# Kernel tuning notes

Hardware: AMD Instinct MI355X
Metric: run time of the kernel (lower is better)

The kernel has to match this reference:

```python
import jax, jax.numpy as jnp
import numpy as np

EMBED_DIM = 512
NUM_HEADS = 8
HEAD_DIM = EMBED_DIM // NUM_HEADS
N_NODES = 65536
EPS = 1e-5


def setup_inputs() -> dict:
    key = jax.random.key(0)
    ks = jax.random.split(key, 16)
    std = 0.02
    E, F = EMBED_DIM, 4 * EMBED_DIM
    return {
        "x": jax.random.normal(ks[0], (N_NODES, E), jnp.float32),
        "Wq": jax.random.normal(ks[1], (E, E), jnp.float32) * std,
        "bq": jnp.zeros((E,), jnp.float32),
        "Wk": jax.random.normal(ks[2], (E, E), jnp.float32) * std,
        "bk": jnp.zeros((E,), jnp.float32),
        "Wv": jax.random.normal(ks[3], (E, E), jnp.float32) * std,
        "bv": jnp.zeros((E,), jnp.float32),
        "Wo": jax.random.normal(ks[4], (E, E), jnp.float32) * std,
        "bo": jnp.zeros((E,), jnp.float32),
        "W1": jax.random.normal(ks[5], (F, E), jnp.float32) * std,
        "b1": jnp.zeros((F,), jnp.float32),
        "W2": jax.random.normal(ks[6], (E, F), jnp.float32) * std,
        "b2": jnp.zeros((E,), jnp.float32),
        "g1": jnp.ones((E,), jnp.float32),
        "beta1": jnp.zeros((E,), jnp.float32),
        "g2": jnp.ones((E,), jnp.float32),
        "beta2": jnp.zeros((E,), jnp.float32),
    }


def _layernorm(x, g, b):
    mu = jnp.mean(x, axis=-1, keepdims=True)
    var = jnp.mean(jnp.square(x - mu), axis=-1, keepdims=True)
    return (x - mu) * jax.lax.rsqrt(var + EPS) * g + b


def reference(x, Wq, bq, Wk, bk, Wv, bv, Wo, bo, W1, b1, W2, b2, g1, beta1, g2, beta2):
    N = x.shape[0]
    H, D = NUM_HEADS, HEAD_DIM
    residual = x
    h = _layernorm(x, g1, beta1)
    q = (h @ Wq.T + bq).reshape(N, H, D)
    k = (h @ Wk.T + bk).reshape(N, H, D)
    v = (h @ Wv.T + bv).reshape(N, H, D)
    # per-node attention across heads: scores (N, H, H)
    scores = jnp.einsum('nhd,ngd->nhg', q, k) / np.float32(np.sqrt(D))
    attn = jax.nn.softmax(scores, axis=-1)
    out = jnp.einsum('nhg,ngd->nhd', attn, v).reshape(N, H * D)
    out = out @ Wo.T + bo
    x = residual + out  # dropout is identity in eval
    residual = x
    h = _layernorm(x, g2, beta2)
    ff = jax.nn.relu(h @ W1.T + b1) @ W2.T + b2
    return residual + ff
```

## Files before the change

### kernel.cpp

```cpp
#include <hip/hip_runtime.h>
#include <hip/hip_bf16.h>
#include <stdint.h>

typedef __hip_bfloat16 bf16;
typedef short bf16x8 __attribute__((ext_vector_type(8)));
typedef float f32x4 __attribute__((ext_vector_type(4)));

typedef __attribute__((address_space(1))) const unsigned int as1_uint;
typedef __attribute__((address_space(3))) unsigned int as3_uint;

__device__ __forceinline__ void async_copy16(const void* g, void* l) {
    __builtin_amdgcn_global_load_lds((as1_uint*)g, (as3_uint*)l, 16, 0, 0);
}

__device__ __forceinline__ float b2f(unsigned short u) {
    union { unsigned int i; float f; } c; c.i = ((unsigned int)u) << 16; return c.f;
}
__device__ __forceinline__ unsigned short f2b(float f) {
    union { float f; unsigned int i; } c; c.f = f;
    unsigned int i = c.i;
    i += 0x7fffu + ((i >> 16) & 1u);
    return (unsigned short)(i >> 16);
}

__global__ __launch_bounds__(256)
void cvt_kernel(const float* __restrict__ in, bf16* __restrict__ out)
{
    const int i = (blockIdx.x * 256 + threadIdx.x) * 8;
    const float4 a = *(const float4*)(in + i);
    const float4 b = *(const float4*)(in + i + 4);
    union { uint4 v; unsigned short s[8]; } u;
    u.s[0] = f2b(a.x); u.s[1] = f2b(a.y); u.s[2] = f2b(a.z); u.s[3] = f2b(a.w);
    u.s[4] = f2b(b.x); u.s[5] = f2b(b.y); u.s[6] = f2b(b.z); u.s[7] = f2b(b.w);
    *(uint4*)((unsigned short*)out + i) = u.v;
}

__global__ __launch_bounds__(256)
void ln_kernel(const float* __restrict__ x, const float* __restrict__ g,
               const float* __restrict__ beta, bf16* __restrict__ out)
{
    const int w = threadIdx.x >> 6, l = threadIdx.x & 63;
    const int n = blockIdx.x * 4 + w;

    const float* xr = x + (size_t)n * 512 + l * 8;
    const float4 a = *(const float4*)xr;
    const float4 b = *(const float4*)(xr + 4);
    float f[8] = {a.x, a.y, a.z, a.w, b.x, b.y, b.z, b.w};

    float s = 0.f, q = 0.f;
#pragma unroll
    for (int i = 0; i < 8; ++i) { s += f[i]; q += f[i] * f[i]; }
#pragma unroll
    for (int o = 32; o > 0; o >>= 1) { s += __shfl_xor(s, o); q += __shfl_xor(q, o); }
    const float mean = s * (1.f / 512.f);
    const float var  = q * (1.f / 512.f) - mean * mean;
    const float rstd = rsqrtf(var + 1e-5f);

    const float4 g0 = *(const float4*)(g + l * 8);
    const float4 g1 = *(const float4*)(g + l * 8 + 4);
    const float4 b0 = *(const float4*)(beta + l * 8);
    const float4 b1 = *(const float4*)(beta + l * 8 + 4);
    const float gg[8] = {g0.x,g0.y,g0.z,g0.w,g1.x,g1.y,g1.z,g1.w};
    const float bb[8] = {b0.x,b0.y,b0.z,b0.w,b1.x,b1.y,b1.z,b1.w};

    union { uint4 v; unsigned short s[8]; } o;
#pragma unroll
    for (int i = 0; i < 8; ++i)
        o.s[i] = f2b((f[i] - mean) * rstd * gg[i] + bb[i]);
    *(uint4*)((unsigned short*)out + (size_t)n * 512 + l * 8) = o.v;
}

__global__ __launch_bounds__(256)
void attn_kernel(const bf16* __restrict__ qkv, bf16* __restrict__ out)
{
    __shared__ unsigned short sm[4][1536];
    const int w = threadIdx.x >> 6, l = threadIdx.x & 63;
    const int n = blockIdx.x * 4 + w;

    const uint4* src = (const uint4*)((const unsigned short*)qkv + (size_t)n * 1536);
    uint4* dst = (uint4*)sm[w];
#pragma unroll
    for (int i = 0; i < 3; ++i) dst[i * 64 + l] = src[i * 64 + l];
    __syncthreads();

    const int h = l >> 3, gi = l & 7;
    const unsigned short* qrow = sm[w] + h * 64;
    const unsigned short* krow = sm[w] + 512 + gi * 64;
    float s = 0.f;
#pragma unroll
    for (int jj = 0; jj < 8; ++jj) {
        union { uint4 v; unsigned short s8[8]; } qa, ka;
        qa.v = *(const uint4*)(qrow + jj * 8);
        ka.v = *(const uint4*)(krow + jj * 8);
#pragma unroll
        for (int j = 0; j < 8; ++j) s += b2f(qa.s8[j]) * b2f(ka.s8[j]);
    }
    s *= 0.125f;

    float m = s;
#pragma unroll
    for (int o = 1; o < 8; o <<= 1) m = fmaxf(m, __shfl_xor(m, o));
    float e = __expf(s - m);
    float d = e;
#pragma unroll
    for (int o = 1; o < 8; o <<= 1) d += __shfl_xor(d, o);
    const float p = e / d;

    float acc[8];
#pragma unroll
    for (int j = 0; j < 8; ++j) acc[j] = 0.f;
    const int j8 = (l & 7) * 8;
#pragma unroll
    for (int gg = 0; gg < 8; ++gg) {
        const float pg = __shfl(p, (l & 56) | gg);
        union { uint4 v; unsigned short s8[8]; } va;
        va.v = *(const uint4*)(sm[w] + 1024 + gg * 64 + j8);
#pragma unroll
        for (int j = 0; j < 8; ++j) acc[j] += pg * b2f(va.s8[j]);
    }
    union { uint4 v; unsigned short s8[8]; } o;
#pragma unroll
    for (int j = 0; j < 8; ++j) o.s8[j] = f2b(acc[j]);
    *(uint4*)((unsigned short*)out + (size_t)n * 512 + h * 64 + j8) = o.v;
}

#define EPI_PLAIN 0
#define EPI_RES   1
#define EPI_RELU  2

template<int MODE>
__global__ __launch_bounds__(256)
void gemm_bt(const bf16* __restrict__ A,
             const bf16* __restrict__ B0, const bf16* __restrict__ B1,
             const bf16* __restrict__ B2,
             const float* __restrict__ bias0, const float* __restrict__ bias1,
             const float* __restrict__ bias2,
             const float* __restrict__ res,
             void* __restrict__ C,
             int K, int Nper, int ldc)
{
    __shared__ bf16 As[128 * 64];
    __shared__ bf16 Bs[128 * 64];

    const int tid = threadIdx.x;
    const int w = tid >> 6, l = tid & 63;
    const int rowBase = blockIdx.y * 128;
    const int colBase = blockIdx.x * 128;
    const int sel = colBase / Nper;
    const bf16*  B    = (sel == 0) ? B0 : (sel == 1) ? B1 : B2;
    const float* bias = (sel == 0) ? bias0 : (sel == 1) ? bias1 : bias2;
    const int colInB = colBase - sel * Nper;

    const int la = l >> 3;
    const int lk = (l & 7) * 8;
    const bf16* Ag = A + (size_t)(rowBase + w * 32 + la) * K + lk;
    const bf16* Bg = B + (size_t)(colInB + w * 32 + la) * K + lk;
    bf16* AsW = As + (w * 32) * 64;
    bf16* BsW = Bs + (w * 32) * 64;

    const int wr = w >> 1, wc = w & 1;
    const int ml = l & 15;
    const int kq = (l >> 4) * 8;

    f32x4 acc[4][4];
#pragma unroll
    for (int i = 0; i < 4; ++i)
#pragma unroll
        for (int j = 0; j < 4; ++j) acc[i][j] = (f32x4)(0.f);

    for (int k0 = 0; k0 < K; k0 += 64) {
#pragma unroll
        for (int i = 0; i < 4; ++i) {
            async_copy16(Ag + (size_t)(i * 8) * K + k0, AsW + i * 8 * 64);
            async_copy16(Bg + (size_t)(i * 8) * K + k0, BsW + i * 8 * 64);
        }
        __syncthreads();
#pragma unroll
        for (int kk = 0; kk < 2; ++kk) {
            const int ko = kk * 32 + kq;
            bf16x8 af[4], bfr[4];
#pragma unroll
            for (int mi = 0; mi < 4; ++mi)
                af[mi] = *(const bf16x8*)(As + (wr * 64 + mi * 16 + ml) * 64 + ko);
#pragma unroll
            for (int ni = 0; ni < 4; ++ni)
                bfr[ni] = *(const bf16x8*)(Bs + (wc * 64 + ni * 16 + ml) * 64 + ko);
#pragma unroll
            for (int mi = 0; mi < 4; ++mi)
#pragma unroll
                for (int ni = 0; ni < 4; ++ni)
                    acc[mi][ni] = __builtin_amdgcn_mfma_f32_16x16x32_bf16(
                        af[mi], bfr[ni], acc[mi][ni], 0, 0, 0);
        }
        __syncthreads();
    }

    float bv[4];
#pragma unroll
    for (int ni = 0; ni < 4; ++ni)
        bv[ni] = bias[colInB + wc * 64 + ni * 16 + ml];

#pragma unroll
    for (int mi = 0; mi < 4; ++mi) {
#pragma unroll
        for (int r = 0; r < 4; ++r) {
            const int row = rowBase + wr * 64 + mi * 16 + (l >> 4) * 4 + r;
            const size_t rowoff = (size_t)row * ldc;
#pragma unroll
            for (int ni = 0; ni < 4; ++ni) {
                const int gcol = colBase + wc * 64 + ni * 16 + ml;
                float v = acc[mi][ni][r] + bv[ni];
                if (MODE == EPI_RELU) v = fmaxf(v, 0.f);
                if (MODE == EPI_RES) {
                    v += res[rowoff + gcol];
                    ((float*)C)[rowoff + gcol] = v;
                } else {
                    ((unsigned short*)C)[rowoff + gcol] = f2b(v);
                }
            }
        }
    }
}

extern "C" void kernel_launch(void* const* d_in, const int* in_sizes, int n_in,
                              void* d_out, int out_size, void* d_ws, size_t ws_size,
                              hipStream_t stream)
{
    const float* x   = (const float*)d_in[0];
    const float* Wq  = (const float*)d_in[1];
    const float* bq  = (const float*)d_in[2];
    const float* Wk  = (const float*)d_in[3];
    const float* bk  = (const float*)d_in[4];
    const float* Wv  = (const float*)d_in[5];
    const float* bv  = (const float*)d_in[6];
    const float* Wo  = (const float*)d_in[7];
    const float* bo  = (const float*)d_in[8];
    const float* W1  = (const float*)d_in[9];
    const float* b1  = (const float*)d_in[10];
    const float* W2  = (const float*)d_in[11];
    const float* b2  = (const float*)d_in[12];
    const float* g1  = (const float*)d_in[13];
    const float* be1 = (const float*)d_in[14];
    const float* g2  = (const float*)d_in[15];
    const float* be2 = (const float*)d_in[16];

    const int N = 65536;

    bf16* Wqb = (bf16*)d_ws;
    bf16* Wkb = Wqb + 262144;
    bf16* Wvb = Wkb + 262144;
    bf16* Wob = Wvb + 262144;
    bf16* W1b = Wob + 262144;
    bf16* W2b = W1b + 1048576;
    const size_t wts_bytes = 6ull * 1024 * 1024;
    bf16* t64 = (bf16*)((char*)d_ws + wts_bytes);
    const size_t t64_bytes = (size_t)N * 512 * 2;
    bf16* cb  = (bf16*)((char*)d_ws + wts_bytes + t64_bytes);
    const size_t used = wts_bytes + t64_bytes;
    const size_t avail = ws_size > used ? ws_size - used : 0;
    int Nc = N;
    while (Nc > 128 && (size_t)Nc * 4096 > avail) Nc >>= 1;

    float* x2 = (float*)d_out;
    dim3 blk(256);

    cvt_kernel<<<262144 / 2048, blk, 0, stream>>>(Wq, Wqb);
    cvt_kernel<<<262144 / 2048, blk, 0, stream>>>(Wk, Wkb);
    cvt_kernel<<<262144 / 2048, blk, 0, stream>>>(Wv, Wvb);
    cvt_kernel<<<262144 / 2048, blk, 0, stream>>>(Wo, Wob);
    cvt_kernel<<<1048576 / 2048, blk, 0, stream>>>(W1, W1b);
    cvt_kernel<<<1048576 / 2048, blk, 0, stream>>>(W2, W2b);

    ln_kernel<<<N / 4, blk, 0, stream>>>(x, g1, be1, t64);

    for (int r0 = 0; r0 < N; r0 += Nc) {
        gemm_bt<EPI_PLAIN><<<dim3(12, Nc / 128), blk, 0, stream>>>(
            t64 + (size_t)r0 * 512, Wqb, Wkb, Wvb, bq, bk, bv, nullptr,
            cb, 512, 512, 1536);
        attn_kernel<<<Nc / 4, blk, 0, stream>>>(cb, t64 + (size_t)r0 * 512);
    }

    gemm_bt<EPI_RES><<<dim3(4, N / 128), blk, 0, stream>>>(
        t64, Wob, Wob, Wob, bo, bo, bo, x, x2, 512, 512, 512);

    ln_kernel<<<N / 4, blk, 0, stream>>>(x2, g2, be2, t64);

    for (int r0 = 0; r0 < N; r0 += Nc) {
        gemm_bt<EPI_RELU><<<dim3(16, Nc / 128), blk, 0, stream>>>(
            t64 + (size_t)r0 * 512, W1b, W1b, W1b, b1, b1, b1, nullptr,
            cb, 512, 2048, 2048);
        gemm_bt<EPI_RES><<<dim3(4, Nc / 128), blk, 0, stream>>>(
            cb, W2b, W2b, W2b, b2, b2, b2, x2 + (size_t)r0 * 512,
            x2 + (size_t)r0 * 512, 2048, 512, 512);
    }
}
```

Before: 1.076 ms.

## Rewrite GEMM as 256x256 tile with 4-stage async LDS pipeline and XCD remap

The bf16 GEMM moves from 128x128 tiles with 4 waves and a single LDS buffer to 256x256 tiles with 8 waves. Global-to-LDS loads run through a 4-slot ring with K-step 32 and a prefetch depth of 3, paced by explicit vmcnt waits, and the LDS layout uses an XOR swizzle to avoid bank conflicts. Workgroup IDs are remapped so neighbouring tiles share an XCD, and MFMA sections raise wave priority. The aim is to hide load latency and raise data reuse, at the cost of more LDS (128KB) and registers per block, and a different chunk size for the host loop.

Result: faster. 1.052 ms (-2.3%).

```diff
diff --git a/kernel.cpp b/kernel.cpp
--- a/kernel.cpp
+++ b/kernel.cpp
@@ -129,7 +129,7 @@
 #define EPI_RELU  2
 
 template<int MODE>
-__global__ __launch_bounds__(256)
+__global__ __launch_bounds__(512, 2)
 void gemm_bt(const bf16* __restrict__ A,
              const bf16* __restrict__ B0, const bf16* __restrict__ B1,
              const bf16* __restrict__ B2,
@@ -139,77 +139,104 @@
              void* __restrict__ C,
              int K, int Nper, int ldc)
 {
-    __shared__ bf16 As[128 * 64];
-    __shared__ bf16 Bs[128 * 64];
+    __shared__ bf16 As[4][8192];
+    __shared__ bf16 Bs[4][8192];
 
     const int tid = threadIdx.x;
     const int w = tid >> 6, l = tid & 63;
-    const int rowBase = blockIdx.y * 128;
-    const int colBase = blockIdx.x * 128;
+
+    const int nbx = gridDim.x;
+    const int nwg = nbx * (int)gridDim.y;
+    int lid = blockIdx.y * nbx + blockIdx.x;
+    {
+        const int q = nwg >> 3, r = nwg & 7;
+        const int xcd = lid & 7, idx = lid >> 3;
+        lid = (xcd < r ? xcd * (q + 1) : r * (q + 1) + (xcd - r) * q) + idx;
+    }
+    const int bx = lid % nbx, by = lid / nbx;
+
+    const int rowBase = by * 256;
+    const int colBase = bx * 256;
     const int sel = colBase / Nper;
     const bf16*  B    = (sel == 0) ? B0 : (sel == 1) ? B1 : B2;
     const float* bias = (sel == 0) ? bias0 : (sel == 1) ? bias1 : bias2;
     const int colInB = colBase - sel * Nper;
 
-    const int la = l >> 3;
-    const int lk = (l & 7) * 8;
-    const bf16* Ag = A + (size_t)(rowBase + w * 32 + la) * K + lk;
-    const bf16* Bg = B + (size_t)(colInB + w * 32 + la) * K + lk;
-    bf16* AsW = As + (w * 32) * 64;
-    bf16* BsW = Bs + (w * 32) * 64;
-
-    const int wr = w >> 1, wc = w & 1;
+    const bf16* Ag = A + (size_t)rowBase * K;
+    const bf16* Bg = B + (size_t)colInB * K;
+
+    const int wr = w >> 2, wc = w & 3;
     const int ml = l & 15;
-    const int kq = (l >> 4) * 8;
-
-    f32x4 acc[4][4];
-#pragma unroll
-    for (int i = 0; i < 4; ++i)
+    const int kc = l >> 4;
+    const int ac = ((kc ^ ((ml >> 1) & 3)) << 3);
+
+    auto stage = [&](int t, int slot) {
+        const int lr = l >> 2, lc = l & 3;
+#pragma unroll
+        for (int j = 0; j < 2; ++j) {
+            const int cid = w * 2 + j;
+            const int r = (cid << 4) + lr;
+            const int c = lc ^ ((lr >> 1) & 3);
+            const size_t go = (size_t)r * K + (t << 5) + (c << 3);
+            async_copy16(Ag + go, &As[slot][cid << 9]);
+            async_copy16(Bg + go, &Bs[slot][cid << 9]);
+        }
+    };
+
+    f32x4 acc[8][4];
+#pragma unroll
+    for (int i = 0; i < 8; ++i)
 #pragma unroll
         for (int j = 0; j < 4; ++j) acc[i][j] = (f32x4)(0.f);
 
-    for (int k0 = 0; k0 < K; k0 += 64) {
-#pragma unroll
-        for (int i = 0; i < 4; ++i) {
-            async_copy16(Ag + (size_t)(i * 8) * K + k0, AsW + i * 8 * 64);
-            async_copy16(Bg + (size_t)(i * 8) * K + k0, BsW + i * 8 * 64);
+    const int NT = K >> 5;
+
+    stage(0, 0); stage(1, 1); stage(2, 2);
+    asm volatile("s_waitcnt vmcnt(8)" ::: "memory");
+    __builtin_amdgcn_s_barrier();
+
+    for (int t = 0; t < NT; ++t) {
+        if (t + 3 < NT) stage(t + 3, (t + 3) & 3);
+
+        const bf16* Ac = &As[t & 3][0];
+        const bf16* Bc = &Bs[t & 3][0];
+        bf16x8 bfr[4];
+#pragma unroll
+        for (int ni = 0; ni < 4; ++ni)
+            bfr[ni] = *(const bf16x8*)(Bc + (((wc << 6) + (ni << 4) + ml) << 5) + ac);
+
+        __builtin_amdgcn_s_setprio(1);
+#pragma unroll
+        for (int mi = 0; mi < 8; ++mi) {
+            const bf16x8 a = *(const bf16x8*)(Ac + (((wr << 7) + (mi << 4) + ml) << 5) + ac);
+#pragma unroll
+            for (int ni = 0; ni < 4; ++ni)
+                acc[mi][ni] = __builtin_amdgcn_mfma_f32_16x16x32_bf16(
+                    a, bfr[ni], acc[mi][ni], 0, 0, 0);
         }
-        __syncthreads();
-#pragma unroll
-        for (int kk = 0; kk < 2; ++kk) {
-            const int ko = kk * 32 + kq;
-            bf16x8 af[4], bfr[4];
-#pragma unroll
-            for (int mi = 0; mi < 4; ++mi)
-                af[mi] = *(const bf16x8*)(As + (wr * 64 + mi * 16 + ml) * 64 + ko);
-#pragma unroll
-            for (int ni = 0; ni < 4; ++ni)
-                bfr[ni] = *(const bf16x8*)(Bs + (wc * 64 + ni * 16 + ml) * 64 + ko);
-#pragma unroll
-            for (int mi = 0; mi < 4; ++mi)
-#pragma unroll
-                for (int ni = 0; ni < 4; ++ni)
-                    acc[mi][ni] = __builtin_amdgcn_mfma_f32_16x16x32_bf16(
-                        af[mi], bfr[ni], acc[mi][ni], 0, 0, 0);
-        }
-        __syncthreads();
+        __builtin_amdgcn_s_setprio(0);
+
+        if (t < NT - 3)       asm volatile("s_waitcnt vmcnt(8)" ::: "memory");
+        else if (t == NT - 3) asm volatile("s_waitcnt vmcnt(4)" ::: "memory");
+        else if (t == NT - 2) asm volatile("s_waitcnt vmcnt(0)" ::: "memory");
+        if (t < NT - 1) __builtin_amdgcn_s_barrier();
     }
 
     float bv[4];
 #pragma unroll
     for (int ni = 0; ni < 4; ++ni)
-        bv[ni] = bias[colInB + wc * 64 + ni * 16 + ml];
-
-#pragma unroll
-    for (int mi = 0; mi < 4; ++mi) {
-#pragma unroll
-        for (int r = 0; r < 4; ++r) {
-            const int row = rowBase + wr * 64 + mi * 16 + (l >> 4) * 4 + r;
+        bv[ni] = bias[colInB + (wc << 6) + (ni << 4) + ml];
+
+#pragma unroll
+    for (int mi = 0; mi < 8; ++mi) {
+#pragma unroll
+        for (int r4 = 0; r4 < 4; ++r4) {
+            const int row = rowBase + (wr << 7) + (mi << 4) + (kc << 2) + r4;
             const size_t rowoff = (size_t)row * ldc;
 #pragma unroll
             for (int ni = 0; ni < 4; ++ni) {
-                const int gcol = colBase + wc * 64 + ni * 16 + ml;
-                float v = acc[mi][ni][r] + bv[ni];
+                const int gcol = colBase + (wc << 6) + (ni << 4) + ml;
+                float v = acc[mi][ni][r4] + bv[ni];
                 if (MODE == EPI_RELU) v = fmaxf(v, 0.f);
                 if (MODE == EPI_RES) {
                     v += res[rowoff + gcol];
@@ -258,11 +285,12 @@
     bf16* cb  = (bf16*)((char*)d_ws + wts_bytes + t64_bytes);
     const size_t used = wts_bytes + t64_bytes;
     const size_t avail = ws_size > used ? ws_size - used : 0;
-    int Nc = N;
-    while (Nc > 128 && (size_t)Nc * 4096 > avail) Nc >>= 1;
+    int Nc = 32768;
+    while (Nc > 256 && (size_t)Nc * 4096 > avail) Nc >>= 1;
 
     float* x2 = (float*)d_out;
     dim3 blk(256);
+    dim3 blk5(512);
 
     cvt_kernel<<<262144 / 2048, blk, 0, stream>>>(Wq, Wqb);
     cvt_kernel<<<262144 / 2048, blk, 0, stream>>>(Wk, Wkb);
@@ -274,22 +302,22 @@
     ln_kernel<<<N / 4, blk, 0, stream>>>(x, g1, be1, t64);
 
     for (int r0 = 0; r0 < N; r0 += Nc) {
-        gemm_bt<EPI_PLAIN><<<dim3(12, Nc / 128), blk, 0, stream>>>(
+        gemm_bt<EPI_PLAIN><<<dim3(6, Nc / 256), blk5, 0, stream>>>(
             t64 + (size_t)r0 * 512, Wqb, Wkb, Wvb, bq, bk, bv, nullptr,
             cb, 512, 512, 1536);
         attn_kernel<<<Nc / 4, blk, 0, stream>>>(cb, t64 + (size_t)r0 * 512);
     }
 
-    gemm_bt<EPI_RES><<<dim3(4, N / 128), blk, 0, stream>>>(
+    gemm_bt<EPI_RES><<<dim3(2, N / 256), blk5, 0, stream>>>(
         t64, Wob, Wob, Wob, bo, bo, bo, x, x2, 512, 512, 512);
 
     ln_kernel<<<N / 4, blk, 0, stream>>>(x2, g2, be2, t64);
 
     for (int r0 = 0; r0 < N; r0 += Nc) {
-        gemm_bt<EPI_RELU><<<dim3(16, Nc / 128), blk, 0, stream>>>(
+        gemm_bt<EPI_RELU><<<dim3(8, Nc / 256), blk5, 0, stream>>>(
             t64 + (size_t)r0 * 512, W1b, W1b, W1b, b1, b1, b1, nullptr,
             cb, 512, 2048, 2048);
-        gemm_bt<EPI_RES><<<dim3(4, Nc / 128), blk, 0, stream>>>(
+        gemm_bt<EPI_RES><<<dim3(2, Nc / 256), blk5, 0, stream>>>(
             cb, W2b, W2b, W2b, b2, b2, b2, x2 + (size_t)r0 * 512,
             x2 + (size_t)r0 * 512, 2048, 512, 512);
     }
```
